# Performance work log

Hardware: AMD Instinct MI355X
Metric: run time of the kernel (lower is better)

The kernel has to match this reference:

```python
import jax, jax.numpy as jnp
import numpy as np

B, T, C, H = 2, 1024, 1024, 16
HD = C // H  # head_dim = 64


def setup_inputs() -> dict:
    key = jax.random.key(0)
    ks = jax.random.split(key, 11)
    s = 0.02  # init scale for weights
    inp = {
        "Q": jax.random.normal(ks[0], (B, T, C), jnp.float32),
        "K": jax.random.normal(ks[1], (B, T, C), jnp.float32),
        "V": jax.random.normal(ks[2], (B, T, C), jnp.float32),
        "Wq": jax.random.normal(ks[3], (C, C), jnp.float32) * s,
        "bq": jnp.zeros((C,), jnp.float32),
        "Wk": jax.random.normal(ks[4], (C, C), jnp.float32) * s,
        "bk": jnp.zeros((C,), jnp.float32),
        "Wv": jax.random.normal(ks[5], (C, C), jnp.float32) * s,
        "bv": jnp.zeros((C,), jnp.float32),
        "Wp": jax.random.normal(ks[6], (C, C), jnp.float32) * s,
        "bp": jax.random.normal(ks[7], (C,), jnp.float32) * s,
        # causal attention mask: True = masked (matches masked_fill semantics)
        "attn_mask": jnp.triu(jnp.ones((T, T), jnp.bool_), k=1),
    }
    return inp


def reference(Q, K, V, Wq, bq, Wk, bk, Wv, bv, Wp, bp, attn_mask):
    b, t, c = Q.shape

    def proj(x, W, bias):
        # nn.Linear: x @ W.T + b, then split heads -> [B, H, T, HD]
        return (x @ W.T + bias).reshape(b, t, H, HD).transpose(0, 2, 1, 3)

    q = proj(Q, Wq, bq)
    k = proj(K, Wk, bk)
    v = proj(V, Wv, bv)
    # scoreF: scaled dot-product -> [B, H, T, T]
    a = jnp.einsum('bhtd,bhsd->bhts', q, k) / jnp.sqrt(jnp.asarray(HD, q.dtype))
    a = jnp.where(attn_mask, -jnp.inf, a)  # masked_fill(attn_mask, -inf)
    a = jax.nn.softmax(a, axis=-1)  # ADropout is identity (p=0)
    y = jnp.einsum('bhts,bhsd->bhtd', a, v)  # a @ v
    y = y.transpose(0, 2, 1, 3).reshape(b, t, c)
    y = y @ Wp.T + bp  # P projection; RDropout identity (p=0)
    return (y, a)
```

## Files before the change

kernel.cpp:

```cpp
#include <hip/hip_runtime.h>
#include <hip/hip_bf16.h>

typedef short bf16x8 __attribute__((ext_vector_type(8)));
typedef float f32x4 __attribute__((ext_vector_type(4)));
typedef unsigned short u16;
typedef u16 u16x8 __attribute__((ext_vector_type(8)));

#define MFMA16(a, b, c) __builtin_amdgcn_mfma_f32_16x16x32_bf16(a, b, c, 0, 0, 0)


__device__ __forceinline__ u16 f2bf(float f) {
    unsigned u = __builtin_bit_cast(unsigned, f);
    unsigned r = (u + 0x7FFFu + ((u >> 16) & 1u)) >> 16;
    return (u16)r;
}

__global__ __launch_bounds__(256) void cvt_bf16(
    const float* __restrict__ Q, const float* __restrict__ K, const float* __restrict__ V,
    const float* __restrict__ Wq, const float* __restrict__ Wk, const float* __restrict__ Wv,
    const float* __restrict__ Wp,
    u16* __restrict__ Qb, u16* __restrict__ Kb, u16* __restrict__ Vb,
    u16* __restrict__ Wqb, u16* __restrict__ Wkb, u16* __restrict__ Wvb,
    u16* __restrict__ Wpb) {
    const int z = blockIdx.y;
    const float* src;
    u16* dst;
    int n;
    switch (z) {
        case 0: src = Q;  dst = Qb;  n = 1 << 21; break;
        case 1: src = K;  dst = Kb;  n = 1 << 21; break;
        case 2: src = V;  dst = Vb;  n = 1 << 21; break;
        case 3: src = Wq; dst = Wqb; n = 1 << 20; break;
        case 4: src = Wk; dst = Wkb; n = 1 << 20; break;
        case 5: src = Wv; dst = Wvb; n = 1 << 20; break;
        default: src = Wp; dst = Wpb; n = 1 << 20; break;
    }
    const int i = (blockIdx.x * 256 + threadIdx.x) * 8;
    if (i >= n) return;
    float4 f0 = *(const float4*)(src + i);
    float4 f1 = *(const float4*)(src + i + 4);
    u16x8 t;
    t[0] = f2bf(f0.x); t[1] = f2bf(f0.y); t[2] = f2bf(f0.z); t[3] = f2bf(f0.w);
    t[4] = f2bf(f1.x); t[5] = f2bf(f1.y); t[6] = f2bf(f1.z); t[7] = f2bf(f1.w);
    *(u16x8*)(dst + i) = t;
}

template <int BM, bool OF32>
__device__ inline void gemm_body(const u16* __restrict__ A,
                                 const u16* __restrict__ W,
                                 const float* __restrict__ bias,
                                 void* __restrict__ outp, int mode) {
    __shared__ u16 As[BM * 64];
    __shared__ u16 Bs[64 * 64];

    const int tid = threadIdx.x;
    const int wave = tid >> 6, lane = tid & 63;
    const int quad = lane >> 4, l16 = lane & 15;
    constexpr int WM = BM / 2;
    constexpr int MI = WM / 16;
    const int wm = (wave >> 1) * WM;
    const int wn = (wave & 1) * 32;
    const int m0 = blockIdx.y * BM;
    const int n0 = blockIdx.x * 64;

    f32x4 acc[MI][2] = {};

    const int lrow = lane >> 3;
    const int lseg = lane & 7;
    const u16* Ag = A + (size_t)(m0 + wave * 8 + lrow) * 1024 + lseg * 8;
    const u16* Wg = W + (size_t)(n0 + wave * 8 + lrow) * 1024 + lseg * 8;
    u16* AsBase = As + wave * 8 * 64;
    u16* BsBase = Bs + wave * 8 * 64;

    for (int kt = 0; kt < 16; ++kt) {
        const int k0 = kt * 64;
        __syncthreads();
#pragma unroll
        for (int rr = 0; rr < BM / 32; ++rr)
            __builtin_amdgcn_global_load_lds(
                (const __attribute__((address_space(1))) void*)(Ag + (size_t)rr * 32 * 1024 + k0),
                (__attribute__((address_space(3))) void*)(AsBase + rr * 32 * 64), 16, 0, 0);
#pragma unroll
        for (int rr = 0; rr < 2; ++rr)
            __builtin_amdgcn_global_load_lds(
                (const __attribute__((address_space(1))) void*)(Wg + (size_t)rr * 32 * 1024 + k0),
                (__attribute__((address_space(3))) void*)(BsBase + rr * 32 * 64), 16, 0, 0);
        __syncthreads();
#pragma unroll
        for (int ks = 0; ks < 2; ++ks) {
            bf16x8 af[MI], bfr[2];
#pragma unroll
            for (int mi = 0; mi < MI; ++mi)
                af[mi] = *(const bf16x8*)(As + (wm + mi * 16 + l16) * 64 + ks * 32 + quad * 8);
#pragma unroll
            for (int ni = 0; ni < 2; ++ni)
                bfr[ni] = *(const bf16x8*)(Bs + (wn + ni * 16 + l16) * 64 + ks * 32 + quad * 8);
#pragma unroll
            for (int mi = 0; mi < MI; ++mi)
#pragma unroll
                for (int ni = 0; ni < 2; ++ni)
                    acc[mi][ni] = MFMA16(af[mi], bfr[ni], acc[mi][ni]);
        }
    }

#pragma unroll
    for (int ni = 0; ni < 2; ++ni) {
        const int n = n0 + wn + ni * 16 + l16;
        const float bv = bias[n];
#pragma unroll
        for (int mi = 0; mi < MI; ++mi) {
#pragma unroll
            for (int r = 0; r < 4; ++r) {
                const int m = m0 + wm + mi * 16 + quad * 4 + r;
                const float val = acc[mi][ni][r] + bv;
                size_t idx;
                if (mode == 0) {
                    int b = m >> 10, t = m & 1023, h = n >> 6, d = n & 63;
                    idx = ((size_t)((b * 16 + h) * 1024 + t)) * 64 + d;
                } else if (mode == 1) {
                    int b = m >> 10, t = m & 1023, h = n >> 6, d = n & 63;
                    idx = ((size_t)((b * 16 + h) * 64 + d)) * 1024 + t;
                } else {
                    idx = (size_t)m * 1024 + n;
                }
                if (OF32) ((float*)outp)[idx] = val;
                else      ((u16*)outp)[idx] = f2bf(val);
            }
        }
    }
}

__global__ __launch_bounds__(256) void proj_qkv(
    const u16* __restrict__ Qb, const u16* __restrict__ Kb, const u16* __restrict__ Vb,
    const u16* __restrict__ Wqb, const u16* __restrict__ Wkb, const u16* __restrict__ Wvb,
    const float* __restrict__ bq, const float* __restrict__ bk, const float* __restrict__ bv,
    u16* __restrict__ q_ws, u16* __restrict__ k_ws, u16* __restrict__ vt_ws) {
    const int z = blockIdx.z;
    const u16* A = (z == 0) ? Qb : (z == 1) ? Kb : Vb;
    const u16* W = (z == 0) ? Wqb : (z == 1) ? Wkb : Wvb;
    const float* bias = (z == 0) ? bq : (z == 1) ? bk : bv;
    u16* out = (z == 0) ? q_ws : (z == 1) ? k_ws : vt_ws;
    gemm_body<128, false>(A, W, bias, out, (z == 2) ? 1 : 0);
}

__global__ __launch_bounds__(256) void proj_out(
    const u16* __restrict__ A, const u16* __restrict__ Wpb,
    const float* __restrict__ bp, float* __restrict__ y) {
    gemm_body<64, true>(A, Wpb, bp, y, 2);
}

__global__ __launch_bounds__(256) void attn_fused(
    const u16* __restrict__ q_ws, const u16* __restrict__ k_ws,
    const u16* __restrict__ vt_ws, float* __restrict__ a_out,
    u16* __restrict__ ao_ws) {
    __shared__ u16 P[4][1024];
    __shared__ float Ls[4][16];
    __shared__ float Osum[4][1024];

    const int tid = threadIdx.x;
    const int wave = tid >> 6, lane = tid & 63;
    const int quad = lane >> 4, l16 = lane & 15;

    const int id = blockIdx.x;
    const int wgid = (id & 7) * 256 + (id >> 3);
    const int bh = wgid >> 6;
    const int strip = 63 - (wgid & 63);
    const int b = bh >> 4, h = bh & 15;
    const int wrow = strip * 16;
    const int nt = (strip >> 2) + 1;

    const u16* qh = q_ws + (size_t)bh * 65536;
    const u16* kh = k_ws + (size_t)bh * 65536;
    const u16* vh = vt_ws + (size_t)bh * 65536;
    float* ah = a_out + ((size_t)bh << 20);

    bf16x8 qf[2];
    qf[0] = *(const bf16x8*)(qh + (size_t)(wrow + l16) * 64 + quad * 8);
    qf[1] = *(const bf16x8*)(qh + (size_t)(wrow + l16) * 64 + 32 + quad * 8);

    float sum_r[4] = {0.f, 0.f, 0.f, 0.f};
    f32x4 o[4] = {};

    for (int s = 0; s < 4; ++s) {
        const int ct = wave + s * 4;
        if (ct < nt) {
            f32x4 c[4] = {};
#pragma unroll
            for (int ks = 0; ks < 2; ++ks)
#pragma unroll
                for (int cb = 0; cb < 4; ++cb) {
                    bf16x8 kf = *(const bf16x8*)(kh + (size_t)(ct * 64 + cb * 16 + l16) * 64 + ks * 32 + quad * 8);
                    c[cb] = MFMA16(qf[ks], kf, c[cb]);
                }
#pragma unroll
            for (int cb = 0; cb < 4; ++cb) {
                const int s_col = cb * 16 + l16;
                const int col = ct * 64 + s_col;
#pragma unroll
                for (int r = 0; r < 4; ++r) {
                    const int m = quad * 4 + r;
                    const int trow = wrow + m;
                    float E = __expf(c[cb][r] * 0.125f - 20.0f);
                    if (col > trow) E = 0.0f;
                    sum_r[r] += E;
                    P[wave][(s_col >> 3) * 128 + m * 8 + (s_col & 7)] = f2bf(E);
                }
            }
#pragma unroll
            for (int ks = 0; ks < 2; ++ks) {
                bf16x8 pf = *(const bf16x8*)(&P[wave][(ks * 4 + quad) * 128 + l16 * 8]);
#pragma unroll
                for (int nb = 0; nb < 4; ++nb) {
                    bf16x8 vf = *(const bf16x8*)(vh + (size_t)(nb * 16 + l16) * 1024 + ct * 64 + ks * 32 + quad * 8);
                    o[nb] = MFMA16(pf, vf, o[nb]);
                }
            }
        }
    }

#pragma unroll
    for (int r = 0; r < 4; ++r) {
#pragma unroll
        for (int off = 1; off < 16; off <<= 1)
            sum_r[r] += __shfl_xor(sum_r[r], off);
    }
    if (l16 == 0) {
#pragma unroll
        for (int r = 0; r < 4; ++r) Ls[wave][quad * 4 + r] = sum_r[r];
    }
    __syncthreads();

    float rl[4];
#pragma unroll
    for (int r = 0; r < 4; ++r) {
        const int m = quad * 4 + r;
        rl[r] = 1.0f / (Ls[0][m] + Ls[1][m] + Ls[2][m] + Ls[3][m]);
    }

#pragma unroll
    for (int nb = 0; nb < 4; ++nb)
#pragma unroll
        for (int r = 0; r < 4; ++r) {
            const int row = quad * 4 + r;
            const int d = nb * 16 + l16;
            Osum[wave][row * 64 + (d ^ ((row >> 2) << 4))] = o[nb][r] * rl[r];
        }

    for (int s = 0; s < 4; ++s) {
        const int ct = wave + s * 4;
        if (ct < nt) {
            f32x4 c[4] = {};
#pragma unroll
            for (int ks = 0; ks < 2; ++ks)
#pragma unroll
                for (int cb = 0; cb < 4; ++cb) {
                    bf16x8 kf = *(const bf16x8*)(kh + (size_t)(ct * 64 + cb * 16 + l16) * 64 + ks * 32 + quad * 8);
                    c[cb] = MFMA16(qf[ks], kf, c[cb]);
                }
#pragma unroll
            for (int cb = 0; cb < 4; ++cb) {
                const int col = ct * 64 + cb * 16 + l16;
#pragma unroll
                for (int r = 0; r < 4; ++r) {
                    const int trow = wrow + quad * 4 + r;
                    float E = __expf(c[cb][r] * 0.125f - 20.0f);
                    if (col > trow) E = 0.0f;
                    __builtin_nontemporal_store(E * rl[r], ah + (size_t)trow * 1024 + col);
                }
            }
        }
    }

    {
        const f32x4 zz = {0.f, 0.f, 0.f, 0.f};
        for (int ct = nt + wave; ct < 16; ct += 4) {
#pragma unroll
            for (int j = 0; j < 4; ++j)
                __builtin_nontemporal_store(
                    zz, (f32x4*)(ah + (size_t)(wrow + j * 4 + quad) * 1024 + ct * 64 + l16 * 4));
        }
    }

    __syncthreads();

#pragma unroll
    for (int i = 0; i < 4; ++i) {
        const int e = tid + i * 256;
        const int row = e >> 6, d = e & 63;
        const int sd = row * 64 + (d ^ ((row >> 2) << 4));
        const float v = Osum[0][sd] + Osum[1][sd] + Osum[2][sd] + Osum[3][sd];
        ao_ws[((size_t)(b * 1024 + wrow + row)) * 1024 + h * 64 + d] = f2bf(v);
    }
}

extern "C" void kernel_launch(void* const* d_in, const int* in_sizes, int n_in,
                              void* d_out, int out_size, void* d_ws, size_t ws_size,
                              hipStream_t stream) {
    const float* Q  = (const float*)d_in[0];
    const float* K  = (const float*)d_in[1];
    const float* V  = (const float*)d_in[2];
    const float* Wq = (const float*)d_in[3];
    const float* bq = (const float*)d_in[4];
    const float* Wk = (const float*)d_in[5];
    const float* bk = (const float*)d_in[6];
    const float* Wv = (const float*)d_in[7];
    const float* bv = (const float*)d_in[8];
    const float* Wp = (const float*)d_in[9];
    const float* bp = (const float*)d_in[10];

    float* y = (float*)d_out;
    float* a = y + (size_t)2 * 1024 * 1024;

    const size_t M1 = (size_t)1 << 20;
    u16* q_ws  = (u16*)d_ws;
    u16* k_ws  = q_ws  + 2 * M1;
    u16* vt_ws = k_ws  + 2 * M1;
    u16* ao_ws = vt_ws + 2 * M1;
    u16* Qb    = ao_ws + 2 * M1;
    u16* Kb    = Qb    + 2 * M1;
    u16* Vb    = Kb    + 2 * M1;
    u16* Wqb   = Vb    + 2 * M1;
    u16* Wkb   = Wqb   + M1;
    u16* Wvb   = Wkb   + M1;
    u16* Wpb   = Wvb   + M1;

    hipLaunchKernelGGL(cvt_bf16, dim3(1024, 7), dim3(256), 0, stream,
                       Q, K, V, Wq, Wk, Wv, Wp, Qb, Kb, Vb, Wqb, Wkb, Wvb, Wpb);
    hipLaunchKernelGGL(proj_qkv, dim3(16, 16, 3), dim3(256), 0, stream,
                       Qb, Kb, Vb, Wqb, Wkb, Wvb, bq, bk, bv, q_ws, k_ws, vt_ws);
    hipLaunchKernelGGL(attn_fused, dim3(2048), dim3(256), 0, stream,
                       q_ws, k_ws, vt_ws, a, ao_ws);
    hipLaunchKernelGGL(proj_out, dim3(16, 32, 1), dim3(256), 0, stream,
                       ao_ws, Wpb, bp, y);
}
```

Before: 275.4 us.

## Reuse stored bf16 probabilities for attention output and widen QKV GEMM tile

The attention kernel now keeps each wave's per-tile unnormalized exp values in shared memory (one buffer per tile) instead of recomputing QK^T and exp in a second pass. After the row sums are known, it writes the normalized probabilities from that buffer with vectorized stores. It also reuses the same shared buffer for the output partial sums. The QKV projection GEMM switches to 128x128 tiles with half the grid. The attention matrix now comes from bf16-rounded probabilities, which lowers its precision, and the larger shared footprint may reduce occupancy.

After: 264.6 us. 3.9% less time.

```diff
diff --git a/kernel.cpp b/kernel.cpp
--- a/kernel.cpp
+++ b/kernel.cpp
@@ -4,6 +4,7 @@
 typedef short bf16x8 __attribute__((ext_vector_type(8)));
 typedef float f32x4 __attribute__((ext_vector_type(4)));
 typedef unsigned short u16;
+typedef u16 u16x4 __attribute__((ext_vector_type(4)));
 typedef u16 u16x8 __attribute__((ext_vector_type(8)));
 
 #define MFMA16(a, b, c) __builtin_amdgcn_mfma_f32_16x16x32_bf16(a, b, c, 0, 0, 0)
@@ -13,6 +14,10 @@
     unsigned u = __builtin_bit_cast(unsigned, f);
     unsigned r = (u + 0x7FFFu + ((u >> 16) & 1u)) >> 16;
     return (u16)r;
+}
+
+__device__ __forceinline__ float bf2f(u16 v) {
+    return __builtin_bit_cast(float, ((unsigned)v) << 16);
 }
 
 __global__ __launch_bounds__(256) void cvt_bf16(
@@ -45,25 +50,27 @@
     *(u16x8*)(dst + i) = t;
 }
 
-template <int BM, bool OF32>
+template <int BM, int BN, bool OF32>
 __device__ inline void gemm_body(const u16* __restrict__ A,
                                  const u16* __restrict__ W,
                                  const float* __restrict__ bias,
                                  void* __restrict__ outp, int mode) {
     __shared__ u16 As[BM * 64];
-    __shared__ u16 Bs[64 * 64];
+    __shared__ u16 Bs[BN * 64];
 
     const int tid = threadIdx.x;
     const int wave = tid >> 6, lane = tid & 63;
     const int quad = lane >> 4, l16 = lane & 15;
     constexpr int WM = BM / 2;
+    constexpr int WN = BN / 2;
     constexpr int MI = WM / 16;
+    constexpr int NI = WN / 16;
     const int wm = (wave >> 1) * WM;
-    const int wn = (wave & 1) * 32;
+    const int wn = (wave & 1) * WN;
     const int m0 = blockIdx.y * BM;
-    const int n0 = blockIdx.x * 64;
-
-    f32x4 acc[MI][2] = {};
+    const int n0 = blockIdx.x * BN;
+
+    f32x4 acc[MI][NI] = {};
 
     const int lrow = lane >> 3;
     const int lseg = lane & 7;
@@ -81,30 +88,30 @@
                 (const __attribute__((address_space(1))) void*)(Ag + (size_t)rr * 32 * 1024 + k0),
                 (__attribute__((address_space(3))) void*)(AsBase + rr * 32 * 64), 16, 0, 0);
 #pragma unroll
-        for (int rr = 0; rr < 2; ++rr)
+        for (int rr = 0; rr < BN / 32; ++rr)
             __builtin_amdgcn_global_load_lds(
                 (const __attribute__((address_space(1))) void*)(Wg + (size_t)rr * 32 * 1024 + k0),
                 (__attribute__((address_space(3))) void*)(BsBase + rr * 32 * 64), 16, 0, 0);
         __syncthreads();
 #pragma unroll
         for (int ks = 0; ks < 2; ++ks) {
-            bf16x8 af[MI], bfr[2];
+            bf16x8 af[MI], bfr[NI];
 #pragma unroll
             for (int mi = 0; mi < MI; ++mi)
                 af[mi] = *(const bf16x8*)(As + (wm + mi * 16 + l16) * 64 + ks * 32 + quad * 8);
 #pragma unroll
-            for (int ni = 0; ni < 2; ++ni)
+            for (int ni = 0; ni < NI; ++ni)
                 bfr[ni] = *(const bf16x8*)(Bs + (wn + ni * 16 + l16) * 64 + ks * 32 + quad * 8);
 #pragma unroll
             for (int mi = 0; mi < MI; ++mi)
 #pragma unroll
-                for (int ni = 0; ni < 2; ++ni)
+                for (int ni = 0; ni < NI; ++ni)
                     acc[mi][ni] = MFMA16(af[mi], bfr[ni], acc[mi][ni]);
         }
     }
 
 #pragma unroll
-    for (int ni = 0; ni < 2; ++ni) {
+    for (int ni = 0; ni < NI; ++ni) {
         const int n = n0 + wn + ni * 16 + l16;
         const float bv = bias[n];
 #pragma unroll
@@ -140,22 +147,22 @@
     const u16* W = (z == 0) ? Wqb : (z == 1) ? Wkb : Wvb;
     const float* bias = (z == 0) ? bq : (z == 1) ? bk : bv;
     u16* out = (z == 0) ? q_ws : (z == 1) ? k_ws : vt_ws;
-    gemm_body<128, false>(A, W, bias, out, (z == 2) ? 1 : 0);
+    gemm_body<128, 128, false>(A, W, bias, out, (z == 2) ? 1 : 0);
 }
 
 __global__ __launch_bounds__(256) void proj_out(
     const u16* __restrict__ A, const u16* __restrict__ Wpb,
     const float* __restrict__ bp, float* __restrict__ y) {
-    gemm_body<64, true>(A, Wpb, bp, y, 2);
+    gemm_body<64, 64, true>(A, Wpb, bp, y, 2);
 }
 
 __global__ __launch_bounds__(256) void attn_fused(
     const u16* __restrict__ q_ws, const u16* __restrict__ k_ws,
     const u16* __restrict__ vt_ws, float* __restrict__ a_out,
     u16* __restrict__ ao_ws) {
-    __shared__ u16 P[4][1024];
+    __shared__ u16 Pall[4][4][1024];
     __shared__ float Ls[4][16];
-    __shared__ float Osum[4][1024];
+    __shared__ float Lrl[16];
 
     const int tid = threadIdx.x;
     const int wave = tid >> 6, lane = tid & 63;
@@ -203,12 +210,12 @@
                     float E = __expf(c[cb][r] * 0.125f - 20.0f);
                     if (col > trow) E = 0.0f;
                     sum_r[r] += E;
-                    P[wave][(s_col >> 3) * 128 + m * 8 + (s_col & 7)] = f2bf(E);
+                    Pall[wave][s][(s_col >> 3) * 128 + m * 8 + (s_col & 7)] = f2bf(E);
                 }
             }
 #pragma unroll
             for (int ks = 0; ks < 2; ++ks) {
-                bf16x8 pf = *(const bf16x8*)(&P[wave][(ks * 4 + quad) * 128 + l16 * 8]);
+                bf16x8 pf = *(const bf16x8*)(&Pall[wave][s][(ks * 4 + quad) * 128 + l16 * 8]);
 #pragma unroll
                 for (int nb = 0; nb < 4; ++nb) {
                     bf16x8 vf = *(const bf16x8*)(vh + (size_t)(nb * 16 + l16) * 1024 + ct * 64 + ks * 32 + quad * 8);
@@ -218,6 +225,16 @@
         }
     }
 
+    {
+        const f32x4 zz = {0.f, 0.f, 0.f, 0.f};
+        for (int ct = nt + wave; ct < 16; ct += 4) {
+#pragma unroll
+            for (int j = 0; j < 4; ++j)
+                __builtin_nontemporal_store(
+                    zz, (f32x4*)(ah + (size_t)(wrow + j * 4 + quad) * 1024 + ct * 64 + l16 * 4));
+        }
+    }
+
 #pragma unroll
     for (int r = 0; r < 4; ++r) {
 #pragma unroll
@@ -236,51 +253,44 @@
         const int m = quad * 4 + r;
         rl[r] = 1.0f / (Ls[0][m] + Ls[1][m] + Ls[2][m] + Ls[3][m]);
     }
-
+    if (wave == 0 && l16 == 0) {
+#pragma unroll
+        for (int r = 0; r < 4; ++r) Lrl[quad * 4 + r] = rl[r];
+    }
+    __syncthreads();
+
+    {
+        const int col4 = l16 * 4;
+        const int kseg = col4 >> 3, koff = col4 & 7;
+        for (int s = 0; s < 4; ++s) {
+            const int ct = wave + s * 4;
+            if (ct < nt) {
+#pragma unroll
+                for (int i = 0; i < 4; ++i) {
+                    const int row = quad + i * 4;
+                    const u16x4 pv = *(const u16x4*)(&Pall[wave][s][kseg * 128 + row * 8 + koff]);
+                    const float rlr = Lrl[row];
+                    f32x4 vv;
+                    vv[0] = bf2f(pv[0]) * rlr;
+                    vv[1] = bf2f(pv[1]) * rlr;
+                    vv[2] = bf2f(pv[2]) * rlr;
+                    vv[3] = bf2f(pv[3]) * rlr;
+                    __builtin_nontemporal_store(
+                        vv, (f32x4*)(ah + (size_t)(wrow + row) * 1024 + ct * 64 + col4));
+                }
+            }
+        }
+    }
+
+    float* Osum_w = (float*)&Pall[wave][0][0];
 #pragma unroll
     for (int nb = 0; nb < 4; ++nb)
 #pragma unroll
         for (int r = 0; r < 4; ++r) {
             const int row = quad * 4 + r;
             const int d = nb * 16 + l16;
-            Osum[wave][row * 64 + (d ^ ((row >> 2) << 4))] = o[nb][r] * rl[r];
-        }
-
-    for (int s = 0; s < 4; ++s) {
-        const int ct = wave + s * 4;
-        if (ct < nt) {
-            f32x4 c[4] = {};
-#pragma unroll
-            for (int ks = 0; ks < 2; ++ks)
-#pragma unroll
-                for (int cb = 0; cb < 4; ++cb) {
-                    bf16x8 kf = *(const bf16x8*)(kh + (size_t)(ct * 64 + cb * 16 + l16) * 64 + ks * 32 + quad * 8);
-                    c[cb] = MFMA16(qf[ks], kf, c[cb]);
-                }
-#pragma unroll
-            for (int cb = 0; cb < 4; ++cb) {
-                const int col = ct * 64 + cb * 16 + l16;
-#pragma unroll
-                for (int r = 0; r < 4; ++r) {
-                    const int trow = wrow + quad * 4 + r;
-                    float E = __expf(c[cb][r] * 0.125f - 20.0f);
-                    if (col > trow) E = 0.0f;
-                    __builtin_nontemporal_store(E * rl[r], ah + (size_t)trow * 1024 + col);
-                }
-            }
-        }
-    }
-
-    {
-        const f32x4 zz = {0.f, 0.f, 0.f, 0.f};
-        for (int ct = nt + wave; ct < 16; ct += 4) {
-#pragma unroll
-            for (int j = 0; j < 4; ++j)
-                __builtin_nontemporal_store(
-                    zz, (f32x4*)(ah + (size_t)(wrow + j * 4 + quad) * 1024 + ct * 64 + l16 * 4));
-        }
-    }
-
+            Osum_w[row * 64 + (d ^ ((row >> 2) << 4))] = o[nb][r] * rl[r];
+        }
     __syncthreads();
 
 #pragma unroll
@@ -288,7 +298,10 @@
         const int e = tid + i * 256;
         const int row = e >> 6, d = e & 63;
         const int sd = row * 64 + (d ^ ((row >> 2) << 4));
-        const float v = Osum[0][sd] + Osum[1][sd] + Osum[2][sd] + Osum[3][sd];
+        float v = 0.f;
+#pragma unroll
+        for (int w = 0; w < 4; ++w)
+            v += ((const float*)&Pall[w][0][0])[sd];
         ao_ws[((size_t)(b * 1024 + wrow + row)) * 1024 + h * 64 + d] = f2bf(v);
     }
 }
@@ -326,7 +339,7 @@
 
     hipLaunchKernelGGL(cvt_bf16, dim3(1024, 7), dim3(256), 0, stream,
                        Q, K, V, Wq, Wk, Wv, Wp, Qb, Kb, Vb, Wqb, Wkb, Wvb, Wpb);
-    hipLaunchKernelGGL(proj_qkv, dim3(16, 16, 3), dim3(256), 0, stream,
+    hipLaunchKernelGGL(proj_qkv, dim3(8, 16, 3), dim3(256), 0, stream,
                        Qb, Kb, Vb, Wqb, Wkb, Wvb, bq, bk, bv, q_ws, k_ws, vt_ws);
     hipLaunchKernelGGL(attn_fused, dim3(2048), dim3(256), 0, stream,
                        q_ws, k_ws, vt_ws, a, ao_ws);
```
